# Performance work log

Hardware: AMD Instinct MI355X
Metric: run time of the kernel (lower is better)

## Reference

```python
import jax, jax.numpy as jnp
import numpy as np

N_BLOCKS = 100
LAYERS_PER_BLOCK = 10
D = 100
D_OUT = 10
BATCH = 65536


def setup_inputs() -> dict:
    key = jax.random.key(0)
    ks = jax.random.split(key, 6)
    bound = 1.0 / np.sqrt(D)  # PyTorch default Linear init bound
    x = jax.random.normal(ks[0], (BATCH, D), dtype=jnp.float32)
    # Stacked weights: [n_blocks, layers_per_block, out, in]
    W = jax.random.uniform(ks[1], (N_BLOCKS, LAYERS_PER_BLOCK, D, D), jnp.float32, -bound, bound)
    b = jax.random.uniform(ks[2], (N_BLOCKS, LAYERS_PER_BLOCK, D), jnp.float32, -bound, bound)
    Wf = jax.random.uniform(ks[3], (D_OUT, D), jnp.float32, -bound, bound)
    bf = jax.random.uniform(ks[4], (D_OUT,), jnp.float32, -bound, bound)
    return {"x": x, "W": W, "b": b, "Wf": Wf, "bf": bf}


def reference(x, W, b, Wf, bf):
    def layer_step(y, wb):
        w, bb = wb  # w: [D, D] (out, in), bb: [D]
        return jax.nn.relu(y @ w.T + bb), None

    def block_step(xb, wb):
        Wb, bb = wb  # [LAYERS_PER_BLOCK, D, D], [LAYERS_PER_BLOCK, D]
        y, _ = jax.lax.scan(layer_step, xb, (Wb, bb))
        return xb + y, None

    out, _ = jax.lax.scan(block_step, x, (W, b))
    return out @ Wf.T + bf
```

## Files before the change

kernel.cpp:

```cpp
#include <hip/hip_runtime.h>
#include <hip/hip_bf16.h>

#define N_LAYERS 1000
#define DD 100
#define DOUT 10
#define FRAG 4096
#define LBYTES (7 * FRAG)
#define NROWS 65536

typedef short s8v __attribute__((ext_vector_type(8)));
typedef float f16v __attribute__((ext_vector_type(16)));
typedef float f4v __attribute__((ext_vector_type(4)));

__device__ __forceinline__ unsigned short f2bf(float f) {
  __hip_bfloat16 h = __float2bfloat16(f);
  return *reinterpret_cast<unsigned short*>(&h);
}
__device__ __forceinline__ float bf2f(unsigned short h) {
  return __uint_as_float(((unsigned)h) << 16);
}
__device__ __forceinline__ unsigned pk2(float a, float b) {
  return (unsigned)f2bf(a) | ((unsigned)f2bf(b) << 16);
}

__global__ __launch_bounds__(256)
void presplit_kernel(const float* __restrict__ W, const float* __restrict__ b,
                     char* __restrict__ hi_g) {
  int idx = blockIdx.x * 256 + threadIdx.x;
  if (idx >= N_LAYERS * 7 * 4 * 64) return;
  int lane = idx & 63;
  int gf = (idx >> 6) & 3;
  int r = idx >> 8;
  int ks = r % 7;
  int L = r / 7;
  int n = gf * 32 + (lane & 31);
  int k0 = ks * 16 + (lane >> 5) * 8;
  s8v hv;
#pragma unroll
  for (int j = 0; j < 8; ++j) {
    int k = k0 + j;
    float v = 0.0f;
    if (n < DD) {
      if (k < DD) v = W[((size_t)L * DD + n) * DD + k];
      else if (k == DD) v = b[(size_t)L * DD + n];
    }
    hv[j] = (short)f2bf(v);
  }
  *(s8v*)(hi_g + (size_t)idx * 16) = hv;
}

__device__ __forceinline__ s8v wconv(int L, int c, int wv, int l31, int lhi,
                                     const float* __restrict__ W_g,
                                     const float* __restrict__ b_g) {
  int n = wv * 32 + l31;
  int k0 = c * 16 + lhi * 8;
  s8v hv;
#pragma unroll
  for (int j = 0; j < 8; ++j) {
    int k = k0 + j;
    float v = 0.0f;
    if (n < DD) {
      if (k < DD) v = W_g[((size_t)L * DD + n) * DD + k];
      else if (k == DD) v = b_g[(size_t)L * DD + n];
    }
    hv[j] = (short)f2bf(v);
  }
  return hv;
}

template <int PRE>
__global__ __launch_bounds__(256, 2)
void resnet_main(const float* __restrict__ x_g,
                 const float* __restrict__ W_g, const float* __restrict__ b_g,
                 const float* __restrict__ Wf_g, const float* __restrict__ bf_g,
                 float* __restrict__ out_g,
                 const char* __restrict__ whi_g, char* __restrict__ xr_g) {
  __shared__ char wbuf[2 * LBYTES];

  const int tid = threadIdx.x;
  const int lane = tid & 63;
  const int wv = tid >> 6;
  const int l31 = lane & 31;
  const int lhi = lane >> 5;
  const int row = blockIdx.x * 128 + wv * 32 + l31;

  s8v bf[7];
#pragma unroll
  for (int ks = 0; ks < 7; ++ks) {
    const int k0 = ks * 16 + lhi * 8;
    unsigned w[4];
#pragma unroll
    for (int p = 0; p < 4; ++p) {
      const int ka = k0 + 2 * p, kb = k0 + 2 * p + 1;
      float a0 = (ka < DD) ? x_g[(size_t)row * DD + ka] : (ka == DD ? 1.0f : 0.0f);
      float a1 = (kb < DD) ? x_g[(size_t)row * DD + kb] : (kb == DD ? 1.0f : 0.0f);
      w[p] = pk2(a0, a1);
    }
    union { s8v v; unsigned u[4]; } t;
    t.u[0] = w[0]; t.u[1] = w[1]; t.u[2] = w[2]; t.u[3] = w[3];
    bf[ks] = t.v;
  }

  f4v xrr[13];
#pragma unroll
  for (int q16 = 0; q16 <= 12; ++q16) {
    const int c0 = 32 * (q16 >> 2) + 8 * (q16 & 3) + 4 * lhi;
    if (c0 < DD) {
      f4v xq;
#pragma unroll
      for (int j = 0; j < 4; ++j) {
        int c = c0 + j;
        xq[j] = (c < DD) ? x_g[(size_t)row * DD + c] : 0.0f;
      }
      if (PRE) *(f4v*)(xr_g + ((size_t)(q16 * 2 + lhi) * NROWS + row) * 16) = xq;
      else xrr[q16] = xq;
    }
  }

#pragma unroll
  for (int c = 0; c < 7; ++c) {
    s8v v;
    if (PRE) v = *(const s8v*)(whi_g + c * FRAG + tid * 16);
    else     v = wconv(0, c, wv, l31, lhi, W_g, b_g);
    *(s8v*)(&wbuf[c * FRAG + tid * 16]) = v;
  }
  __syncthreads();

  f16v zro;
#pragma unroll
  for (int r = 0; r < 16; ++r) zro[r] = 0.0f;

  int cur = 0;
  for (int L = 0; L < N_LAYERS; ++L) {
    const bool more = (L + 1 < N_LAYERS);

    s8v stg[7];
    if (more) {
      if (PRE) {
        const char* ps = whi_g + (size_t)(L + 1) * LBYTES + tid * 16;
#pragma unroll
        for (int c = 0; c < 7; ++c) stg[c] = *(const s8v*)(ps + c * FRAG);
      } else {
#pragma unroll
        for (int c = 0; c < 7; ++c) stg[c] = wconv(L + 1, c, wv, l31, lhi, W_g, b_g);
      }
    }

    const char* rb = &wbuf[cur * LBYTES] + lane * 16;
    s8v wr[2][4];
#pragma unroll
    for (int g = 0; g < 4; ++g) wr[0][g] = *(const s8v*)(rb + g * 1024);
    f16v acc[4];
#pragma unroll
    for (int ks = 0; ks < 7; ++ks) {
      const int s = ks & 1;
      if (ks < 6) {
#pragma unroll
        for (int g = 0; g < 4; ++g)
          wr[s ^ 1][g] = *(const s8v*)(rb + (ks + 1) * FRAG + g * 1024);
      }
      if (ks == 0) {
#pragma unroll
        for (int g = 0; g < 4; ++g)
          acc[g] = __builtin_amdgcn_mfma_f32_32x32x16_bf16(wr[0][g], bf[0], zro, 0, 0, 0);
      } else {
#pragma unroll
        for (int g = 0; g < 4; ++g)
          acc[g] = __builtin_amdgcn_mfma_f32_32x32x16_bf16(wr[s][g], bf[ks], acc[g], 0, 0, 0);
      }
    }

    const bool bend = ((L % 10) == 9);
#pragma unroll
    for (int ks = 0; ks < 7; ++ks) {
      const int g = ks >> 1, qa = 2 * (ks & 1);
      unsigned pa[2], pb[2];
#pragma unroll
      for (int t = 0; t < 2; ++t) {
        const int q = qa + t;
        float o0 = fmaxf(acc[g][4 * q + 0], 0.0f);
        float o1 = fmaxf(acc[g][4 * q + 1], 0.0f);
        float o2 = fmaxf(acc[g][4 * q + 2], 0.0f);
        float o3 = fmaxf(acc[g][4 * q + 3], 0.0f);
        if (bend) {
          const int q16 = g * 4 + q;
          const int c0 = 32 * g + 8 * q + 4 * lhi;
          if (c0 < DD) {
            if (PRE) {
              char* xp = xr_g + ((size_t)(q16 * 2 + lhi) * NROWS + row) * 16;
              f4v xq = *(const f4v*)xp;
              o0 += xq[0]; o1 += xq[1]; o2 += xq[2]; o3 += xq[3];
              f4v nv; nv[0] = o0; nv[1] = o1; nv[2] = o2; nv[3] = o3;
              *(f4v*)xp = nv;
            } else {
              f4v xq = xrr[q16];
              o0 += xq[0]; o1 += xq[1]; o2 += xq[2]; o3 += xq[3];
              f4v nv; nv[0] = o0; nv[1] = o1; nv[2] = o2; nv[3] = o3;
              xrr[q16] = nv;
            }
          }
        }
        pa[t] = pk2(o0, o1); pb[t] = pk2(o2, o3);
      }
      auto rA = __builtin_amdgcn_permlane32_swap((int)pa[0], (int)pa[1], false, false);
      auto rB = __builtin_amdgcn_permlane32_swap((int)pb[0], (int)pb[1], false, false);
      union { s8v v; unsigned u[4]; } t2;
      t2.u[0] = (unsigned)rA[0];
      t2.u[1] = (unsigned)rB[0];
      t2.u[2] = (ks == 6) ? 0x3F80u : (unsigned)rA[1];
      t2.u[3] = (unsigned)rB[1];
      bf[ks] = t2.v;
    }

    if (more) {
      char* wd = &wbuf[(cur ^ 1) * LBYTES] + tid * 16;
#pragma unroll
      for (int c = 0; c < 7; ++c) *(s8v*)(wd + c * FRAG) = stg[c];
    }
    __syncthreads();
    cur ^= 1;
  }

  __syncthreads();
  float* xsf = (float*)wbuf;
  for (int i = tid; i < DOUT * DD; i += 256) xsf[i] = Wf_g[i];
  __syncthreads();

  float part[DOUT];
#pragma unroll
  for (int o = 0; o < DOUT; ++o) part[o] = 0.0f;
#pragma unroll
  for (int ks = 0; ks < 7; ++ks) {
#pragma unroll
    for (int j = 0; j < 8; ++j) {
      const int k = ks * 16 + lhi * 8 + j;
      if (k < DD) {
        float a = bf2f((unsigned short)bf[ks][j]);
#pragma unroll
        for (int o = 0; o < DOUT; ++o) part[o] += a * xsf[o * DD + k];
      }
    }
  }
#pragma unroll
  for (int o = 0; o < DOUT; ++o) part[o] += __shfl_xor(part[o], 32);
  if (lhi == 0) {
#pragma unroll
    for (int o = 0; o < DOUT; ++o)
      out_g[(size_t)row * DOUT + o] = part[o] + bf_g[o];
  }
}

extern "C" void kernel_launch(void* const* d_in, const int* in_sizes, int n_in,
                              void* d_out, int out_size, void* d_ws, size_t ws_size,
                              hipStream_t stream) {
  const float* x = (const float*)d_in[0];
  const float* W = (const float*)d_in[1];
  const float* b = (const float*)d_in[2];
  const float* Wf = (const float*)d_in[3];
  const float* bf = (const float*)d_in[4];
  float* out = (float*)d_out;

  const size_t wpack = (size_t)N_LAYERS * LBYTES;
  const size_t xrbytes = (size_t)25 * NROWS * 16;
  const size_t need = wpack + xrbytes;
  const int nwg = 65536 / 128;
  if (ws_size >= need) {
    char* whi = (char*)d_ws;
    char* xr = whi + wpack;
    const int chunks = N_LAYERS * 7 * 4 * 64;
    presplit_kernel<<<(chunks + 255) / 256, 256, 0, stream>>>(W, b, whi);
    resnet_main<1><<<nwg, 256, 0, stream>>>(x, W, b, Wf, bf, out, whi, xr);
  } else {
    resnet_main<0><<<nwg, 256, 0, stream>>>(x, W, b, Wf, bf, out, nullptr, nullptr);
  }
}
```

Before: 2.163 ms.

## Use 512-thread workgroups sharing weight tiles and keep residual in registers

Doubles the workgroup to 8 waves covering 256 rows, so each layer's bf16 weight tile staged in LDS is shared by twice as many rows and per-row weight traffic from global memory is halved. The cooperative weight copy is redistributed over 512 threads in flat chunks. The residual copy of x, which the PRE path previously spilled to a global workspace and reread at each block end, now always lives in registers. In exchange, register pressure rises under the 512x2 launch bound, and the grid shrinks to 256 workgroups, which may leave some compute units underused.

```diff
diff --git a/kernel.cpp b/kernel.cpp
--- a/kernel.cpp
+++ b/kernel.cpp
@@ -6,7 +6,7 @@
 #define DOUT 10
 #define FRAG 4096
 #define LBYTES (7 * FRAG)
-#define NROWS 65536
+#define NCHUNK 1792
 
 typedef short s8v __attribute__((ext_vector_type(8)));
 typedef float f16v __attribute__((ext_vector_type(16)));
@@ -49,11 +49,15 @@
   *(s8v*)(hi_g + (size_t)idx * 16) = hv;
 }
 
-__device__ __forceinline__ s8v wconv(int L, int c, int wv, int l31, int lhi,
-                                     const float* __restrict__ W_g,
-                                     const float* __restrict__ b_g) {
-  int n = wv * 32 + l31;
-  int k0 = c * 16 + lhi * 8;
+__device__ __forceinline__ s8v wconv_chunk(int L, int c,
+                                           const float* __restrict__ W_g,
+                                           const float* __restrict__ b_g) {
+  int ks = c >> 8;
+  int r = c & 255;
+  int gf = r >> 6;
+  int ln = r & 63;
+  int n = gf * 32 + (ln & 31);
+  int k0 = ks * 16 + (ln >> 5) * 8;
   s8v hv;
 #pragma unroll
   for (int j = 0; j < 8; ++j) {
@@ -69,12 +73,12 @@
 }
 
 template <int PRE>
-__global__ __launch_bounds__(256, 2)
+__global__ __launch_bounds__(512, 2)
 void resnet_main(const float* __restrict__ x_g,
                  const float* __restrict__ W_g, const float* __restrict__ b_g,
                  const float* __restrict__ Wf_g, const float* __restrict__ bf_g,
                  float* __restrict__ out_g,
-                 const char* __restrict__ whi_g, char* __restrict__ xr_g) {
+                 const char* __restrict__ whi_g) {
   __shared__ char wbuf[2 * LBYTES];
 
   const int tid = threadIdx.x;
@@ -82,7 +86,7 @@
   const int wv = tid >> 6;
   const int l31 = lane & 31;
   const int lhi = lane >> 5;
-  const int row = blockIdx.x * 128 + wv * 32 + l31;
+  const int row = blockIdx.x * 256 + wv * 32 + l31;
 
   s8v bf[7];
 #pragma unroll
@@ -105,24 +109,24 @@
 #pragma unroll
   for (int q16 = 0; q16 <= 12; ++q16) {
     const int c0 = 32 * (q16 >> 2) + 8 * (q16 & 3) + 4 * lhi;
-    if (c0 < DD) {
-      f4v xq;
-#pragma unroll
-      for (int j = 0; j < 4; ++j) {
-        int c = c0 + j;
-        xq[j] = (c < DD) ? x_g[(size_t)row * DD + c] : 0.0f;
-      }
-      if (PRE) *(f4v*)(xr_g + ((size_t)(q16 * 2 + lhi) * NROWS + row) * 16) = xq;
-      else xrr[q16] = xq;
-    }
-  }
-
-#pragma unroll
-  for (int c = 0; c < 7; ++c) {
-    s8v v;
-    if (PRE) v = *(const s8v*)(whi_g + c * FRAG + tid * 16);
-    else     v = wconv(0, c, wv, l31, lhi, W_g, b_g);
-    *(s8v*)(&wbuf[c * FRAG + tid * 16]) = v;
+    f4v xq;
+#pragma unroll
+    for (int j = 0; j < 4; ++j) {
+      int c = c0 + j;
+      xq[j] = (c < DD) ? x_g[(size_t)row * DD + c] : 0.0f;
+    }
+    xrr[q16] = xq;
+  }
+
+#pragma unroll
+  for (int i = 0; i < 4; ++i) {
+    const int c = tid + i * 512;
+    if (c < NCHUNK) {
+      s8v v;
+      if (PRE) v = *(const s8v*)(whi_g + (size_t)c * 16);
+      else     v = wconv_chunk(0, c, W_g, b_g);
+      *(s8v*)(&wbuf[c * 16]) = v;
+    }
   }
   __syncthreads();
 
@@ -134,15 +138,15 @@
   for (int L = 0; L < N_LAYERS; ++L) {
     const bool more = (L + 1 < N_LAYERS);
 
-    s8v stg[7];
+    s8v stg[4];
     if (more) {
-      if (PRE) {
-        const char* ps = whi_g + (size_t)(L + 1) * LBYTES + tid * 16;
-#pragma unroll
-        for (int c = 0; c < 7; ++c) stg[c] = *(const s8v*)(ps + c * FRAG);
-      } else {
-#pragma unroll
-        for (int c = 0; c < 7; ++c) stg[c] = wconv(L + 1, c, wv, l31, lhi, W_g, b_g);
+#pragma unroll
+      for (int i = 0; i < 4; ++i) {
+        const int c = tid + i * 512;
+        if (c < NCHUNK) {
+          if (PRE) stg[i] = *(const s8v*)(whi_g + (size_t)(L + 1) * LBYTES + (size_t)c * 16);
+          else     stg[i] = wconv_chunk(L + 1, c, W_g, b_g);
+        }
       }
     }
 
@@ -185,19 +189,11 @@
         if (bend) {
           const int q16 = g * 4 + q;
           const int c0 = 32 * g + 8 * q + 4 * lhi;
-          if (c0 < DD) {
-            if (PRE) {
-              char* xp = xr_g + ((size_t)(q16 * 2 + lhi) * NROWS + row) * 16;
-              f4v xq = *(const f4v*)xp;
-              o0 += xq[0]; o1 += xq[1]; o2 += xq[2]; o3 += xq[3];
-              f4v nv; nv[0] = o0; nv[1] = o1; nv[2] = o2; nv[3] = o3;
-              *(f4v*)xp = nv;
-            } else {
-              f4v xq = xrr[q16];
-              o0 += xq[0]; o1 += xq[1]; o2 += xq[2]; o3 += xq[3];
-              f4v nv; nv[0] = o0; nv[1] = o1; nv[2] = o2; nv[3] = o3;
-              xrr[q16] = nv;
-            }
+          if (q16 <= 12 && c0 < DD) {
+            f4v xq = xrr[q16];
+            o0 += xq[0]; o1 += xq[1]; o2 += xq[2]; o3 += xq[3];
+            f4v nv; nv[0] = o0; nv[1] = o1; nv[2] = o2; nv[3] = o3;
+            xrr[q16] = nv;
           }
         }
         pa[t] = pk2(o0, o1); pb[t] = pk2(o2, o3);
@@ -213,9 +209,11 @@
     }
 
     if (more) {
-      char* wd = &wbuf[(cur ^ 1) * LBYTES] + tid * 16;
-#pragma unroll
-      for (int c = 0; c < 7; ++c) *(s8v*)(wd + c * FRAG) = stg[c];
+#pragma unroll
+      for (int i = 0; i < 4; ++i) {
+        const int c = tid + i * 512;
+        if (c < NCHUNK) *(s8v*)(&wbuf[(cur ^ 1) * LBYTES + c * 16]) = stg[i];
+      }
     }
     __syncthreads();
     cur ^= 1;
@@ -223,7 +221,7 @@
 
   __syncthreads();
   float* xsf = (float*)wbuf;
-  for (int i = tid; i < DOUT * DD; i += 256) xsf[i] = Wf_g[i];
+  for (int i = tid; i < DOUT * DD; i += 512) xsf[i] = Wf_g[i];
   __syncthreads();
 
   float part[DOUT];
@@ -260,17 +258,14 @@
   const float* bf = (const float*)d_in[4];
   float* out = (float*)d_out;
 
-  const size_t wpack = (size_t)N_LAYERS * LBYTES;
-  const size_t xrbytes = (size_t)25 * NROWS * 16;
-  const size_t need = wpack + xrbytes;
-  const int nwg = 65536 / 128;
+  const size_t need = (size_t)N_LAYERS * LBYTES;
+  const int nwg = 65536 / 256;
   if (ws_size >= need) {
     char* whi = (char*)d_ws;
-    char* xr = whi + wpack;
     const int chunks = N_LAYERS * 7 * 4 * 64;
     presplit_kernel<<<(chunks + 255) / 256, 256, 0, stream>>>(W, b, whi);
-    resnet_main<1><<<nwg, 256, 0, stream>>>(x, W, b, Wf, bf, out, whi, xr);
+    resnet_main<1><<<nwg, 512, 0, stream>>>(x, W, b, Wf, bf, out, whi);
   } else {
-    resnet_main<0><<<nwg, 256, 0, stream>>>(x, W, b, Wf, bf, out, nullptr, nullptr);
-  }
-}
+    resnet_main<0><<<nwg, 512, 0, stream>>>(x, W, b, Wf, bf, out, nullptr);
+  }
+}
```

Result: slower. 2.616 ms (+20.9%).
